# Optimization experiments

Measured on AMD Instinct MI355X. Metric: run time of the kernel, lower is better.

Reference implementation:

```python
import jax, jax.numpy as jnp
import numpy as np

LN_EPS = 1e-6

def _layernorm(x, g, b):
    mu = jnp.mean(x, axis=-1, keepdims=True)
    var = jnp.mean((x - mu) ** 2, axis=-1, keepdims=True)
    return (x - mu) / jnp.sqrt(var + LN_EPS) * g + b

def _mha(q, k, v, wq, bq, wk, bk, wv, bv, fc, fcb, ln_g, ln_b, n_head, d_k, d_v):
    # standard post-LN multi-head attention (residual + layernorm), eval mode (no dropout)
    b, lq, _ = q.shape
    bk_, lk, _ = k.shape
    residual = q
    qh = (q @ wq + bq).reshape(b, lq, n_head, d_k).transpose(0, 2, 1, 3)      # [b,h,lq,dk]
    kh = (k @ wk + bk).reshape(bk_, lk, n_head, d_k).transpose(0, 2, 1, 3)    # [bk,h,lk,dk]
    vh = (v @ wv + bv).reshape(bk_, lk, n_head, d_v).transpose(0, 2, 1, 3)    # [bk,h,lk,dv]
    attn = jax.nn.softmax(jnp.matmul(qh, kh.swapaxes(-1, -2)) / (d_k ** 0.5), axis=-1)  # [b,h,lq,lk]
    out = jnp.matmul(attn, vh)                                                # [b,h,lq,dv]
    out = out.transpose(0, 2, 1, 3).reshape(b, lq, n_head * d_v)
    pre = out
    out = _layernorm(out @ fc + fcb + residual, ln_g, ln_b)
    return out, attn, pre


def setup_inputs() -> dict:
    key = jax.random.key(0)
    ks = jax.random.split(key, 32)
    B, C, H, W = 16, 64, 32, 32
    NC, D = 5, 96  # num_classes, memory feature dim
    s = 0.05
    d = {
        'x': jax.random.normal(ks[0], (B, C, H, W), jnp.float32),
        'memory': jax.random.normal(ks[1], (NC, D), jnp.float32),
        'wb_w': jax.random.normal(ks[2], (C, NC), jnp.float32) * s,
        'wb_b': jnp.zeros((NC,), jnp.float32),
        # slf_attn: n_head=1, d_model=64, d_input_k=96, d_k=96, d_v=64
        'a1_wq': jax.random.normal(ks[3], (64, 96), jnp.float32) * s,
        'a1_bq': jnp.zeros((96,), jnp.float32),
        'a1_wk': jax.random.normal(ks[4], (96, 96), jnp.float32) * s,
        'a1_bk': jnp.zeros((96,), jnp.float32),
        'a1_wv': jax.random.normal(ks[5], (96, 64), jnp.float32) * s,
        'a1_bv': jnp.zeros((64,), jnp.float32),
        'a1_fc': jax.random.normal(ks[6], (64, 64), jnp.float32) * s,
        'a1_fcb': jnp.zeros((64,), jnp.float32),
        'a1_ln_g': jnp.ones((64,), jnp.float32),
        'a1_ln_b': jnp.zeros((64,), jnp.float32),
        # slf_attn1: n_head=4, d_model=64, d_input_k=64, d_k=64, d_v=64
        'a2_wq': jax.random.normal(ks[7], (64, 256), jnp.float32) * s,
        'a2_bq': jnp.zeros((256,), jnp.float32),
        'a2_wk': jax.random.normal(ks[8], (64, 256), jnp.float32) * s,
        'a2_bk': jnp.zeros((256,), jnp.float32),
        'a2_wv': jax.random.normal(ks[9], (64, 256), jnp.float32) * s,
        'a2_bv': jnp.zeros((256,), jnp.float32),
        'a2_fc': jax.random.normal(ks[10], (256, 64), jnp.float32) * s,
        'a2_fcb': jnp.zeros((64,), jnp.float32),
        'a2_ln_g': jnp.ones((64,), jnp.float32),
        'a2_ln_b': jnp.zeros((64,), jnp.float32),
    }
    return d


def reference(x, memory, wb_w, wb_b,
              a1_wq, a1_bq, a1_wk, a1_bk, a1_wv, a1_bv, a1_fc, a1_fcb, a1_ln_g, a1_ln_b,
              a2_wq, a2_bq, a2_wk, a2_bk, a2_wv, a2_bv, a2_fc, a2_fcb, a2_ln_g, a2_ln_b):
    b, c, H, W = x.shape
    xt = x.transpose(0, 2, 3, 1).reshape(b, H * W, c)            # [b,HW,64]
    weight = xt @ wb_w + wb_b                                    # [b,HW,5]
    weight1 = jax.nn.softmax(weight, axis=-1)                    # softmax over classes
    weight2 = jax.nn.softmax(weight.transpose(0, 2, 1), axis=-1) # [b,5,HW], softmax over HW
    class_feat1 = jnp.matmul(weight2, xt)                        # [b,5,64] class-weighted pooling
    mem = memory[None]                                           # [1,5,96]
    cf, _, _ = _mha(class_feat1, mem, mem,
                    a1_wq, a1_bq, a1_wk, a1_bk, a1_wv, a1_bv, a1_fc, a1_fcb, a1_ln_g, a1_ln_b,
                    n_head=1, d_k=96, d_v=64)                    # [b,5,64]
    cf = jnp.matmul(weight1, cf)                                 # redistribution [b,HW,64]
    cf, _, _ = _mha(cf, cf, cf,
                    a2_wq, a2_bq, a2_wk, a2_bk, a2_wv, a2_bv, a2_fc, a2_fcb, a2_ln_g, a2_ln_b,
                    n_head=4, d_k=64, d_v=64)                    # [b,HW,64]
    return cf.transpose(0, 2, 1).reshape(-1, 64, H, W)           # [b,64,H,W]
```

## Files before the change

kernel.cpp:

```cpp
#include <hip/hip_runtime.h>
#include <math.h>

typedef unsigned short ushort_t;
typedef __attribute__((ext_vector_type(8))) short short8;
typedef __attribute__((ext_vector_type(4))) float f32x4;

#define B_  16
#define HW_ 1024
#define C_  64
#define NC_ 5
#define D1_ 96
#define NH_ 4
#define DH_ 64

#define MFMA32(A,B,C) __builtin_amdgcn_mfma_f32_16x16x32_bf16(A,B,C,0,0,0)

__device__ __forceinline__ ushort_t f2bf(float f) {
    unsigned u = __float_as_uint(f);
    u = u + 0x7fffu + ((u >> 16) & 1u);
    return (ushort_t)(u >> 16);
}

__device__ __forceinline__ unsigned pack2_trunc(float lo, float hi) {
    return (__float_as_uint(hi) & 0xffff0000u) | (__float_as_uint(lo) >> 16);
}
__device__ __forceinline__ unsigned pack2_rne(float lo, float hi) {
    return ((unsigned)f2bf(hi) << 16) | (unsigned)f2bf(lo);
}
__device__ __forceinline__ float bf_lo(unsigned u) { return __uint_as_float(u << 16); }
__device__ __forceinline__ float bf_hi(unsigned u) { return __uint_as_float(u & 0xffff0000u); }

__device__ __forceinline__ void gload16(const ushort_t* g, ushort_t* l) {
    __builtin_amdgcn_global_load_lds(
        (const __attribute__((address_space(1))) unsigned int*)g,
        (__attribute__((address_space(3))) unsigned int*)l,
        16, 0, 0);
}

__global__ __launch_bounds__(256) void k0_fcT(const float* __restrict__ fc,
                                              ushort_t* __restrict__ F) {
    int c = blockIdx.x * 256 + threadIdx.x;
    int l = c & 63, s = (c >> 6) & 7, n = c >> 9;
    int col = n * 16 + (l & 15);
    int k0 = s * 32 + (l >> 4) * 8;
    union { ushort_t us[8]; uint4 u; } pk;
#pragma unroll
    for (int j = 0; j < 8; j++) pk.us[j] = f2bf(fc[(k0 + j) * 64 + col]);
    *(uint4*)(F + (size_t)c * 8) = pk.u;
}

__global__ __launch_bounds__(256) void k1_logits(const float* __restrict__ x,
                                                 const float* __restrict__ wb_w,
                                                 const float* __restrict__ wb_b,
                                                 float* __restrict__ logitsT,
                                                 float* __restrict__ w1) {
    __shared__ float part[4][64][6];
    int t = threadIdx.x, w = t >> 6, lane = t & 63;
    int b = blockIdx.x >> 4;
    int hw = (blockIdx.x & 15) * 64 + lane;
    const float* xb = x + ((size_t)b * C_ + w * 16) * HW_;
    float acc[NC_] = {0.f, 0.f, 0.f, 0.f, 0.f};
#pragma unroll
    for (int c = 0; c < 16; c++) {
        float xv = xb[c * HW_ + hw];
        const float* wp = wb_w + (w * 16 + c) * NC_;
#pragma unroll
        for (int j = 0; j < NC_; j++) acc[j] += xv * wp[j];
    }
#pragma unroll
    for (int j = 0; j < NC_; j++) part[w][lane][j] = acc[j];
    __syncthreads();
    if (w == 0) {
        float a[NC_];
#pragma unroll
        for (int j = 0; j < NC_; j++)
            a[j] = wb_b[j] + acc[j] + part[1][lane][j] + part[2][lane][j] + part[3][lane][j];
        float m = a[0];
#pragma unroll
        for (int j = 1; j < NC_; j++) m = fmaxf(m, a[j]);
        float e[NC_], s = 0.f;
#pragma unroll
        for (int j = 0; j < NC_; j++) { e[j] = __expf(a[j] - m); s += e[j]; }
        float inv = 1.f / s;
        int idx = b * HW_ + hw;
#pragma unroll
        for (int j = 0; j < NC_; j++) {
            logitsT[((size_t)b * NC_ + j) * HW_ + hw] = a[j];
            w1[(size_t)idx * NC_ + j] = e[j] * inv;
        }
    }
}

__global__ __launch_bounds__(256) void k2b_pool(const float* __restrict__ x,
                                                const float* __restrict__ logitsT,
                                                float* __restrict__ cf1) {
    __shared__ float pl[NC_ * HW_];
    __shared__ float sinv[NC_];
    int t = threadIdx.x;
    int b = blockIdx.x >> 4, chg = blockIdx.x & 15;
    const float* lp = logitsT + (size_t)b * NC_ * HW_;
    for (int i = t * 4; i < NC_ * HW_; i += 1024)
        *(float4*)(pl + i) = *(const float4*)(lp + i);
    __syncthreads();
    int w = t >> 6, lane = t & 63;
    for (int r = w; r < NC_; r += 4) {
        float m = -1e30f;
        for (int i = lane; i < HW_; i += 64) m = fmaxf(m, pl[r * HW_ + i]);
#pragma unroll
        for (int off = 1; off < 64; off <<= 1) m = fmaxf(m, __shfl_xor(m, off, 64));
        float s = 0.f;
        for (int i = lane; i < HW_; i += 64) {
            float e = __expf(pl[r * HW_ + i] - m);
            pl[r * HW_ + i] = e;
            s += e;
        }
#pragma unroll
        for (int off = 1; off < 64; off <<= 1) s += __shfl_xor(s, off, 64);
        if (lane == 0) sinv[r] = 1.f / s;
    }
    __syncthreads();
    int ch = chg * 4 + w;
    const float* xc = x + ((size_t)b * C_ + ch) * HW_;
    float acc[NC_] = {0.f, 0.f, 0.f, 0.f, 0.f};
#pragma unroll
    for (int i = 0; i < HW_ / 64; i++) {
        int hw = i * 64 + lane;
        float xv = xc[hw];
#pragma unroll
        for (int c = 0; c < NC_; c++) acc[c] += xv * pl[c * HW_ + hw];
    }
#pragma unroll
    for (int c = 0; c < NC_; c++) {
        float a = acc[c];
#pragma unroll
        for (int off = 1; off < 64; off <<= 1) a += __shfl_xor(a, off, 64);
        if (lane == 0) cf1[((size_t)b * NC_ + c) * C_ + ch] = a * sinv[c];
    }
}

__global__ __launch_bounds__(256) void k3_mha1(const float* __restrict__ cf1,
                                               const float* __restrict__ wq, const float* __restrict__ bq,
                                               const float* __restrict__ mem,
                                               const float* __restrict__ wk, const float* __restrict__ bk,
                                               const float* __restrict__ wv, const float* __restrict__ bv,
                                               const float* __restrict__ fc, const float* __restrict__ fcb,
                                               const float* __restrict__ lng, const float* __restrict__ lnb,
                                               float* __restrict__ cfs) {
    __shared__ float cs[NC_ * C_];
    __shared__ float kh[NC_ * D1_];
    __shared__ float vh[NC_ * DH_];
    __shared__ float q[NC_ * D1_];
    __shared__ float sc[NC_ * NC_];
    __shared__ float pp[NC_ * NC_];
    __shared__ float o[NC_ * C_];
    __shared__ float z[NC_ * C_];
    __shared__ float mu[NC_], rs[NC_];
    int t = threadIdx.x, b = blockIdx.x;
    for (int i = t; i < NC_ * C_; i += 256) cs[i] = cf1[(size_t)b * NC_ * C_ + i];
    for (int idx = t; idx < NC_ * D1_; idx += 256) {
        int i = idx / D1_, k = idx % D1_;
        float a = bk[k];
        for (int d = 0; d < D1_; d++) a += mem[i * D1_ + d] * wk[d * D1_ + k];
        kh[idx] = a;
    }
    for (int idx = t; idx < NC_ * DH_; idx += 256) {
        int i = idx / DH_, dv = idx % DH_;
        float a = bv[dv];
        for (int d = 0; d < D1_; d++) a += mem[i * D1_ + d] * wv[d * DH_ + dv];
        vh[idx] = a;
    }
    __syncthreads();
    for (int idx = t; idx < NC_ * D1_; idx += 256) {
        int i = idx / D1_, k = idx % D1_;
        float a = bq[k];
        for (int c = 0; c < C_; c++) a += cs[i * C_ + c] * wq[c * D1_ + k];
        q[idx] = a;
    }
    __syncthreads();
    if (t < NC_ * NC_) {
        int i = t / NC_, j = t % NC_;
        float a = 0.f;
        for (int k = 0; k < D1_; k++) a += q[i * D1_ + k] * kh[j * D1_ + k];
        sc[t] = a * 0.1020620726159657f;
    }
    __syncthreads();
    if (t < NC_) {
        float m = sc[t * NC_];
        for (int j = 1; j < NC_; j++) m = fmaxf(m, sc[t * NC_ + j]);
        float e[NC_], s = 0.f;
        for (int j = 0; j < NC_; j++) { e[j] = __expf(sc[t * NC_ + j] - m); s += e[j]; }
        float inv = 1.f / s;
        for (int j = 0; j < NC_; j++) pp[t * NC_ + j] = e[j] * inv;
    }
    __syncthreads();
    for (int idx = t; idx < NC_ * C_; idx += 256) {
        int i = idx / C_, dv = idx % C_;
        float a = 0.f;
        for (int j = 0; j < NC_; j++) a += pp[i * NC_ + j] * vh[j * C_ + dv];
        o[idx] = a;
    }
    __syncthreads();
    for (int idx = t; idx < NC_ * C_; idx += 256) {
        int i = idx / C_, dd = idx % C_;
        float a = fcb[dd] + cs[idx];
        for (int c2 = 0; c2 < C_; c2++) a += o[i * C_ + c2] * fc[c2 * C_ + dd];
        z[idx] = a;
    }
    __syncthreads();
    if (t < NC_) {
        float s = 0.f;
        for (int d = 0; d < C_; d++) s += z[t * C_ + d];
        float mm = s / C_;
        float v = 0.f;
        for (int d = 0; d < C_; d++) { float dd2 = z[t * C_ + d] - mm; v += dd2 * dd2; }
        mu[t] = mm; rs[t] = rsqrtf(v / C_ + 1e-6f);
    }
    __syncthreads();
    for (int idx = t; idx < NC_ * C_; idx += 256) {
        int i = idx / C_, dd = idx % C_;
        cfs[(size_t)b * NC_ * C_ + idx] = (z[idx] - mu[i]) * rs[i] * lng[dd] + lnb[dd];
    }
}

__global__ __launch_bounds__(256) void k5_mfma(const float* __restrict__ w1,
                                               const float* __restrict__ cfs,
                                               const float* __restrict__ wq, const float* __restrict__ bq,
                                               const float* __restrict__ wk, const float* __restrict__ bk,
                                               const float* __restrict__ wv, const float* __restrict__ bv,
                                               ushort_t* __restrict__ Qb, ushort_t* __restrict__ Kb,
                                               ushort_t* __restrict__ Vt) {
    __shared__ ushort_t Af[64][68];
    __shared__ ushort_t Wt[256][68];
    int t = threadIdx.x;
    int which = blockIdx.y;
    int m0 = blockIdx.x * 64;
    int b = m0 >> 10, lbase = m0 & 1023;
    {
        int r = t >> 2, ks = (t & 3) * 16;
        const float* cp = cfs + (size_t)b * NC_ * C_;
        const float* w1p = w1 + (size_t)(m0 + r) * NC_;
        float v0 = w1p[0], v1 = w1p[1], v2 = w1p[2], v3 = w1p[3], v4 = w1p[4];
#pragma unroll
        for (int j = 0; j < 16; j += 2) {
            int k = ks + j;
            float e0 = v0 * cp[k]       + v1 * cp[64 + k]     + v2 * cp[128 + k]
                     + v3 * cp[192 + k] + v4 * cp[256 + k];
            float e1 = v0 * cp[k + 1]     + v1 * cp[64 + k + 1] + v2 * cp[128 + k + 1]
                     + v3 * cp[192 + k + 1] + v4 * cp[256 + k + 1];
            *(unsigned*)&Af[r][k] = pack2_rne(e0, e1);
        }
    }
    const float* W = (which == 0) ? wq : (which == 1) ? wk : wv;
    {
        int n = t;
#pragma unroll
        for (int k = 0; k < 64; k += 2) {
            *(unsigned*)&Wt[n][k] = pack2_rne(W[k * 256 + n], W[(k + 1) * 256 + n]);
        }
    }
    __syncthreads();
    int lane = t & 63, w = t >> 6;
    int l15 = lane & 15, quad = lane >> 4;
    if (which < 2) {
        const float* bias = (which == 0) ? bq : bk;
        float scale = (which == 0) ? 0.18033688011112042f : 1.0f;
        ushort_t* dst = (which == 0) ? Qb : Kb;
        short8 a0[4], a1[4];
#pragma unroll
        for (int mi = 0; mi < 4; mi++) {
            a0[mi] = *(const short8*)&Af[mi * 16 + l15][quad * 8];
            a1[mi] = *(const short8*)&Af[mi * 16 + l15][32 + quad * 8];
        }
#pragma unroll
        for (int nt = 0; nt < 4; nt++) {
            int ni = w * 4 + nt;
            short8 b0 = *(const short8*)&Wt[ni * 16 + l15][quad * 8];
            short8 b1 = *(const short8*)&Wt[ni * 16 + l15][32 + quad * 8];
            int n = ni * 16 + l15;
            float bb = bias[n];
            int h = n >> 6, dd = n & 63;
#pragma unroll
            for (int mi = 0; mi < 4; mi++) {
                f32x4 z = {0, 0, 0, 0};
                f32x4 dv4 = MFMA32(a0[mi], b0, z);
                dv4 = MFMA32(a1[mi], b1, dv4);
                size_t base = ((size_t)(b * NH_ + h) * HW_ + (lbase + mi * 16 + quad * 4)) * DH_ + dd;
#pragma unroll
                for (int r = 0; r < 4; r++)
                    dst[base + (size_t)r * DH_] = f2bf((dv4[r] + bb) * scale);
            }
        }
    } else {
        short8 a0[4], a1[4];
#pragma unroll
        for (int mt = 0; mt < 4; mt++) {
            int mi = w * 4 + mt;
            a0[mt] = *(const short8*)&Wt[mi * 16 + l15][quad * 8];
            a1[mt] = *(const short8*)&Wt[mi * 16 + l15][32 + quad * 8];
        }
#pragma unroll
        for (int nt = 0; nt < 4; nt++) {
            short8 b0 = *(const short8*)&Af[nt * 16 + l15][quad * 8];
            short8 b1 = *(const short8*)&Af[nt * 16 + l15][32 + quad * 8];
#pragma unroll
            for (int mt = 0; mt < 4; mt++) {
                int mi = w * 4 + mt;
                f32x4 z = {0, 0, 0, 0};
                f32x4 dv4 = MFMA32(a0[mt], b0, z);
                dv4 = MFMA32(a1[mt], b1, dv4);
                int h = mi >> 2;
#pragma unroll
                for (int r = 0; r < 4; r++) {
                    int nw = mi * 16 + quad * 4 + r;
                    int dv = nw & 63;
                    Vt[((size_t)(b * NH_ + h) * DH_ + dv) * HW_ + lbase + nt * 16 + l15] =
                        f2bf(dv4[r] + bv[nw]);
                }
            }
        }
    }
}

__global__ __launch_bounds__(256) void k6_attn(const ushort_t* __restrict__ Qb,
                                               const ushort_t* __restrict__ Kb,
                                               const ushort_t* __restrict__ Vt,
                                               ushort_t* __restrict__ aoP0, ushort_t* __restrict__ aoP1,
                                               float* __restrict__ sP0, float* __restrict__ sP1) {
    __shared__ ushort_t Kst[2][8][512];
    int t = threadIdx.x;
    int w = t >> 6;
    int lane = t & 63;
    int l15 = lane & 15;
    int quad = lane >> 4;
    int L = blockIdx.x;
    int bh = ((L >> 3) & 7) * 8 + (L & 7);
    int khalf = (L >> 6) & 1;
    int qt = L >> 7;
    int b = bh >> 2, h = bh & 3;
    const ushort_t* Qp = Qb + (size_t)bh * HW_ * DH_;
    const ushort_t* Kp = Kb + (size_t)bh * HW_ * DH_;
    const ushort_t* Vp = Vt + (size_t)bh * DH_ * HW_;
    int row0 = qt * 256 + w * 16;
    short8 q0[4], q1[4];
#pragma unroll
    for (int tl = 0; tl < 4; tl++) {
        const ushort_t* qp = Qp + (size_t)(row0 + tl * 64 + l15) * DH_ + quad * 8;
        q0[tl] = *(const short8*)(qp);
        q1[tl] = *(const short8*)(qp + 32);
    }
    int f0 = ((l15 >> 2) * 8) + (l15 & 3);
    int kstart = khalf * 512;
    const ushort_t* K0p = Kp + (size_t)(kstart + f0) * DH_ + quad * 8;
    const ushort_t* K1p = Kp + (size_t)(kstart + f0 + 4) * DH_ + quad * 8;
    const ushort_t* Vp0 = Vp + (size_t)(0 * 16 + l15) * HW_ + kstart + quad * 8;
    const ushort_t* Vp1 = Vp + (size_t)(1 * 16 + l15) * HW_ + kstart + quad * 8;
    const ushort_t* Vp2 = Vp + (size_t)(2 * 16 + l15) * HW_ + kstart + quad * 8;
    const ushort_t* Vp3 = Vp + (size_t)(3 * 16 + l15) * HW_ + kstart + quad * 8;
    auto stage = [&](int kt, int bb) {
        size_t koff = (size_t)kt * 32 * DH_;
        int kb32 = kt * 32;
        if (w == 0) {
            gload16(K0p + koff,      &Kst[bb][0][0]);
            gload16(K0p + koff + 32, &Kst[bb][1][0]);
        } else if (w == 1) {
            gload16(K1p + koff,      &Kst[bb][2][0]);
            gload16(K1p + koff + 32, &Kst[bb][3][0]);
        } else if (w == 2) {
            gload16(Vp0 + kb32, &Kst[bb][4][0]);
            gload16(Vp1 + kb32, &Kst[bb][5][0]);
        } else {
            gload16(Vp2 + kb32, &Kst[bb][6][0]);
            gload16(Vp3 + kb32, &Kst[bb][7][0]);
        }
    };
    const short ONE = (short)0x3F80;
    short8 ones = {ONE, ONE, ONE, ONE, ONE, ONE, ONE, ONE};
    f32x4 o0[4], o1[4], o2[4], o3[4], oS[4];
#pragma unroll
    for (int tl = 0; tl < 4; tl++) {
        o0[tl] = (f32x4){0,0,0,0}; o1[tl] = (f32x4){0,0,0,0};
        o2[tl] = (f32x4){0,0,0,0}; o3[tl] = (f32x4){0,0,0,0};
        oS[tl] = (f32x4){0,0,0,0};
    }
    stage(0, 0);
    for (int kt = 0; kt < 16; kt++) {
        int bb = kt & 1;
        __syncthreads();
        if (kt < 15) stage(kt + 1, bb ^ 1);
        const ushort_t* S = &Kst[bb][0][0];
        short8 ka0 = *(const short8*)(S + 0 * 512 + lane * 8);
        short8 ka1 = *(const short8*)(S + 1 * 512 + lane * 8);
        short8 kb0 = *(const short8*)(S + 2 * 512 + lane * 8);
        short8 kb1 = *(const short8*)(S + 3 * 512 + lane * 8);
        short8 v0  = *(const short8*)(S + 4 * 512 + lane * 8);
        short8 v1  = *(const short8*)(S + 5 * 512 + lane * 8);
        short8 v2  = *(const short8*)(S + 6 * 512 + lane * 8);
        short8 v3  = *(const short8*)(S + 7 * 512 + lane * 8);
        f32x4 z = {0,0,0,0};
#pragma unroll
        for (int tl = 0; tl < 4; tl++) {
            f32x4 s0 = MFMA32(ka0, q0[tl], z);  s0 = MFMA32(ka1, q1[tl], s0);
            f32x4 s1 = MFMA32(kb0, q0[tl], z);  s1 = MFMA32(kb1, q1[tl], s1);
            float p0 = exp2f(s0[0]), p1 = exp2f(s0[1]), p2 = exp2f(s0[2]), p3 = exp2f(s0[3]);
            float p4 = exp2f(s1[0]), p5 = exp2f(s1[1]), p6 = exp2f(s1[2]), p7 = exp2f(s1[3]);
            union { short8 v; unsigned u[4]; } pf;
            pf.u[0] = pack2_trunc(p0, p1);  pf.u[1] = pack2_trunc(p2, p3);
            pf.u[2] = pack2_trunc(p4, p5);  pf.u[3] = pack2_trunc(p6, p7);
            o0[tl] = MFMA32(v0, pf.v, o0[tl]);
            o1[tl] = MFMA32(v1, pf.v, o1[tl]);
            o2[tl] = MFMA32(v2, pf.v, o2[tl]);
            o3[tl] = MFMA32(v3, pf.v, o3[tl]);
            oS[tl] = MFMA32(ones, pf.v, oS[tl]);
        }
    }
    ushort_t* aoP = khalf ? aoP1 : aoP0;
    float* sP = khalf ? sP1 : sP0;
#pragma unroll
    for (int tl = 0; tl < 4; tl++) {
        int rowg = row0 + tl * 64 + l15;
        ushort_t* aop = aoP + ((size_t)(b * HW_ + rowg)) * 256 + h * 64 + quad * 4;
        uint2 u;
        u.x = pack2_trunc(o0[tl][0], o0[tl][1]); u.y = pack2_trunc(o0[tl][2], o0[tl][3]);
        *(uint2*)(aop + 0) = u;
        u.x = pack2_trunc(o1[tl][0], o1[tl][1]); u.y = pack2_trunc(o1[tl][2], o1[tl][3]);
        *(uint2*)(aop + 16) = u;
        u.x = pack2_trunc(o2[tl][0], o2[tl][1]); u.y = pack2_trunc(o2[tl][2], o2[tl][3]);
        *(uint2*)(aop + 32) = u;
        u.x = pack2_trunc(o3[tl][0], o3[tl][1]); u.y = pack2_trunc(o3[tl][2], o3[tl][3]);
        *(uint2*)(aop + 48) = u;
        if (quad == 0)
            sP[(size_t)(b * HW_ + rowg) * NH_ + h] = oS[tl][0];
    }
}

__global__ __launch_bounds__(256) void k7_final(const ushort_t* __restrict__ aoP0,
                                                const ushort_t* __restrict__ aoP1,
                                                const float* __restrict__ sP0,
                                                const float* __restrict__ sP1,
                                                const float* __restrict__ w1,
                                                const float* __restrict__ cfs,
                                                const ushort_t* __restrict__ F,
                                                const float* __restrict__ fcb,
                                                const float* __restrict__ lng, const float* __restrict__ lnb,
                                                float* __restrict__ out) {
    __shared__ ushort_t Afr[512 * 8];
    __shared__ float rinv[64];
    __shared__ float T[16][68];
    __shared__ float To[64 * 17];
    int t = threadIdx.x, w = t >> 6, lane = t & 63;
    int m0 = blockIdx.x * 16, b = m0 >> 10;
    if (t < 64) {
        int row = t >> 2, hh = t & 3;
        float s = sP0[(size_t)(m0 + row) * NH_ + hh] + sP1[(size_t)(m0 + row) * NH_ + hh];
        rinv[t] = 1.f / s;
    }
    __syncthreads();
#pragma unroll
    for (int cc = t; cc < 512; cc += 256) {
        int s = cc >> 6, l = cc & 63;
        int row = l & 15, col0 = s * 32 + (l >> 4) * 8;
        int hh = col0 >> 6;
        size_t base = (size_t)(m0 + row) * 256 + col0;
        uint4 a = *(const uint4*)(aoP0 + base);
        uint4 c4 = *(const uint4*)(aoP1 + base);
        float r = rinv[row * 4 + hh];
        uint4 pk;
        pk.x = pack2_trunc((bf_lo(a.x) + bf_lo(c4.x)) * r, (bf_hi(a.x) + bf_hi(c4.x)) * r);
        pk.y = pack2_trunc((bf_lo(a.y) + bf_lo(c4.y)) * r, (bf_hi(a.y) + bf_hi(c4.y)) * r);
        pk.z = pack2_trunc((bf_lo(a.z) + bf_lo(c4.z)) * r, (bf_hi(a.z) + bf_hi(c4.z)) * r);
        pk.w = pack2_trunc((bf_lo(a.w) + bf_lo(c4.w)) * r, (bf_hi(a.w) + bf_hi(c4.w)) * r);
        *(uint4*)&Afr[(size_t)cc * 8] = pk;
    }
    __syncthreads();
    f32x4 acc = {0, 0, 0, 0};
#pragma unroll
    for (int s = 0; s < 8; s++) {
        short8 a = *(const short8*)&Afr[(s * 64 + lane) * 8];
        short8 bf8 = *(const short8*)(F + ((size_t)(w * 8 + s) * 64 + lane) * 8);
        acc = MFMA32(a, bf8, acc);
    }
    {
        int l15 = lane & 15, quad = lane >> 4;
#pragma unroll
        for (int r = 0; r < 4; r++) T[quad * 4 + r][w * 16 + l15] = acc[r];
    }
    __syncthreads();
    int d = lane;
    float g = lng[d], be = lnb[d], bias = fcb[d];
    const float* cp = cfs + (size_t)b * NC_ * C_;
#pragma unroll
    for (int j = 0; j < 4; j++) {
        int row = w * 4 + j;
        const float* w1p = w1 + (size_t)(m0 + row) * NC_;
        float a = bias + T[row][d];
#pragma unroll
        for (int c = 0; c < NC_; c++) a += w1p[c] * cp[c * 64 + d];
        float s1 = a, s2 = a * a;
#pragma unroll
        for (int off = 1; off < 64; off <<= 1) {
            s1 += __shfl_xor(s1, off, 64);
            s2 += __shfl_xor(s2, off, 64);
        }
        float mu = s1 * (1.f / 64.f);
        float var = s2 * (1.f / 64.f) - mu * mu;
        float rstd = rsqrtf(var + 1e-6f);
        To[d * 17 + row] = (a - mu) * rstd * g + be;
    }
    __syncthreads();
    int ch = t >> 2, part = t & 3;
    int hw0 = m0 & 1023;
    float4 v = {To[ch * 17 + part * 4 + 0], To[ch * 17 + part * 4 + 1],
                To[ch * 17 + part * 4 + 2], To[ch * 17 + part * 4 + 3]};
    *(float4*)&out[((size_t)b * 64 + ch) * 1024 + hw0 + part * 4] = v;
}

extern "C" void kernel_launch(void* const* d_in, const int* in_sizes, int n_in,
                              void* d_out, int out_size, void* d_ws, size_t ws_size,
                              hipStream_t stream) {
    const float* x      = (const float*)d_in[0];
    const float* memory = (const float*)d_in[1];
    const float* wb_w   = (const float*)d_in[2];
    const float* wb_b   = (const float*)d_in[3];
    const float* a1_wq  = (const float*)d_in[4];
    const float* a1_bq  = (const float*)d_in[5];
    const float* a1_wk  = (const float*)d_in[6];
    const float* a1_bk  = (const float*)d_in[7];
    const float* a1_wv  = (const float*)d_in[8];
    const float* a1_bv  = (const float*)d_in[9];
    const float* a1_fc  = (const float*)d_in[10];
    const float* a1_fcb = (const float*)d_in[11];
    const float* a1_ln_g = (const float*)d_in[12];
    const float* a1_ln_b = (const float*)d_in[13];
    const float* a2_wq  = (const float*)d_in[14];
    const float* a2_bq  = (const float*)d_in[15];
    const float* a2_wk  = (const float*)d_in[16];
    const float* a2_bk  = (const float*)d_in[17];
    const float* a2_wv  = (const float*)d_in[18];
    const float* a2_bv  = (const float*)d_in[19];
    const float* a2_fc  = (const float*)d_in[20];
    const float* a2_fcb = (const float*)d_in[21];
    const float* a2_ln_g = (const float*)d_in[22];
    const float* a2_ln_b = (const float*)d_in[23];

    float* ws = (float*)d_ws;
    float* logitsT = ws;
    float* w1  = logitsT + 81920;
    float* cf1 = w1 + 81920;
    float* cfs = cf1 + 5120;
    float* sP0 = cfs + 5120;
    float* sP1 = sP0 + 65536;
    ushort_t* aoP0 = (ushort_t*)(sP1 + 65536);
    ushort_t* aoP1 = aoP0 + 4194304;
    ushort_t* Qb = aoP1 + 4194304;
    ushort_t* Kb = Qb + 4194304;
    ushort_t* Vt = Kb + 4194304;
    ushort_t* F  = Vt + 4194304;

    k0_fcT<<<8, 256, 0, stream>>>(a2_fc, F);
    k1_logits<<<256, 256, 0, stream>>>(x, wb_w, wb_b, logitsT, w1);
    k2b_pool<<<256, 256, 0, stream>>>(x, logitsT, cf1);
    k3_mha1<<<16, 256, 0, stream>>>(cf1, a1_wq, a1_bq, memory, a1_wk, a1_bk,
                                    a1_wv, a1_bv, a1_fc, a1_fcb,
                                    a1_ln_g, a1_ln_b, cfs);
    k5_mfma<<<dim3(256, 3), 256, 0, stream>>>(w1, cfs, a2_wq, a2_bq, a2_wk, a2_bk,
                                              a2_wv, a2_bv, Qb, Kb, Vt);
    k6_attn<<<512, 256, 0, stream>>>(Qb, Kb, Vt, aoP0, aoP1, sP0, sP1);
    k7_final<<<1024, 256, 0, stream>>>(aoP0, aoP1, sP0, sP1, w1, cfs, F, a2_fcb,
                                       a2_ln_g, a2_ln_b, (float*)d_out);
}
```

Before: 187.0 us.

## Split attention keys into four chunks and fold small prep kernels into logits launch

The attention kernel now splits the key dimension into four quarters instead of two, doubling the grid to 1024 blocks so more CUs are busy. Each block handles half as many key tiles. The final kernel sums four partial outputs and softmax denominators instead of two. Separately, the fc transpose kernel and the memory K/V projections (previously recomputed in every k3 block) are folded into extra blocks of the logits launch, removing one launch and redundant work. This costs twice the partial-output write and read traffic in the combine step.

```diff
diff --git a/kernel.cpp b/kernel.cpp
--- a/kernel.cpp
+++ b/kernel.cpp
@@ -37,25 +37,47 @@
         16, 0, 0);
 }
 
-__global__ __launch_bounds__(256) void k0_fcT(const float* __restrict__ fc,
-                                              ushort_t* __restrict__ F) {
-    int c = blockIdx.x * 256 + threadIdx.x;
-    int l = c & 63, s = (c >> 6) & 7, n = c >> 9;
-    int col = n * 16 + (l & 15);
-    int k0 = s * 32 + (l >> 4) * 8;
-    union { ushort_t us[8]; uint4 u; } pk;
-#pragma unroll
-    for (int j = 0; j < 8; j++) pk.us[j] = f2bf(fc[(k0 + j) * 64 + col]);
-    *(uint4*)(F + (size_t)c * 8) = pk.u;
-}
-
 __global__ __launch_bounds__(256) void k1_logits(const float* __restrict__ x,
                                                  const float* __restrict__ wb_w,
                                                  const float* __restrict__ wb_b,
+                                                 const float* __restrict__ fc2,
+                                                 const float* __restrict__ mem,
+                                                 const float* __restrict__ wk, const float* __restrict__ bk,
+                                                 const float* __restrict__ wv, const float* __restrict__ bv,
                                                  float* __restrict__ logitsT,
-                                                 float* __restrict__ w1) {
+                                                 float* __restrict__ w1,
+                                                 ushort_t* __restrict__ F,
+                                                 float* __restrict__ khG, float* __restrict__ vhG) {
+    int t = threadIdx.x;
+    if (blockIdx.x >= 256) {
+        int xb2 = blockIdx.x - 256;
+        if (xb2 < 8) {
+            int c = xb2 * 256 + t;
+            int l = c & 63, s = (c >> 6) & 7, n = c >> 9;
+            int col = n * 16 + (l & 15);
+            int k0 = s * 32 + (l >> 4) * 8;
+            union { ushort_t us[8]; uint4 u; } pk;
+#pragma unroll
+            for (int j = 0; j < 8; j++) pk.us[j] = f2bf(fc2[(k0 + j) * 64 + col]);
+            *(uint4*)(F + (size_t)c * 8) = pk.u;
+        } else {
+            for (int idx = t; idx < NC_ * D1_; idx += 256) {
+                int i = idx / D1_, k = idx % D1_;
+                float a = bk[k];
+                for (int d = 0; d < D1_; d++) a += mem[i * D1_ + d] * wk[d * D1_ + k];
+                khG[idx] = a;
+            }
+            for (int idx = t; idx < NC_ * DH_; idx += 256) {
+                int i = idx / DH_, dv = idx % DH_;
+                float a = bv[dv];
+                for (int d = 0; d < D1_; d++) a += mem[i * D1_ + d] * wv[d * DH_ + dv];
+                vhG[idx] = a;
+            }
+        }
+        return;
+    }
     __shared__ float part[4][64][6];
-    int t = threadIdx.x, w = t >> 6, lane = t & 63;
+    int w = t >> 6, lane = t & 63;
     int b = blockIdx.x >> 4;
     int hw = (blockIdx.x & 15) * 64 + lane;
     const float* xb = x + ((size_t)b * C_ + w * 16) * HW_;
@@ -140,9 +162,7 @@
 
 __global__ __launch_bounds__(256) void k3_mha1(const float* __restrict__ cf1,
                                                const float* __restrict__ wq, const float* __restrict__ bq,
-                                               const float* __restrict__ mem,
-                                               const float* __restrict__ wk, const float* __restrict__ bk,
-                                               const float* __restrict__ wv, const float* __restrict__ bv,
+                                               const float* __restrict__ khG, const float* __restrict__ vhG,
                                                const float* __restrict__ fc, const float* __restrict__ fcb,
                                                const float* __restrict__ lng, const float* __restrict__ lnb,
                                                float* __restrict__ cfs) {
@@ -157,18 +177,8 @@
     __shared__ float mu[NC_], rs[NC_];
     int t = threadIdx.x, b = blockIdx.x;
     for (int i = t; i < NC_ * C_; i += 256) cs[i] = cf1[(size_t)b * NC_ * C_ + i];
-    for (int idx = t; idx < NC_ * D1_; idx += 256) {
-        int i = idx / D1_, k = idx % D1_;
-        float a = bk[k];
-        for (int d = 0; d < D1_; d++) a += mem[i * D1_ + d] * wk[d * D1_ + k];
-        kh[idx] = a;
-    }
-    for (int idx = t; idx < NC_ * DH_; idx += 256) {
-        int i = idx / DH_, dv = idx % DH_;
-        float a = bv[dv];
-        for (int d = 0; d < D1_; d++) a += mem[i * D1_ + d] * wv[d * DH_ + dv];
-        vh[idx] = a;
-    }
+    for (int idx = t; idx < NC_ * D1_; idx += 256) kh[idx] = khG[idx];
+    for (int idx = t; idx < NC_ * DH_; idx += 256) vh[idx] = vhG[idx];
     __syncthreads();
     for (int idx = t; idx < NC_ * D1_; idx += 256) {
         int i = idx / D1_, k = idx % D1_;
@@ -324,8 +334,8 @@
 __global__ __launch_bounds__(256) void k6_attn(const ushort_t* __restrict__ Qb,
                                                const ushort_t* __restrict__ Kb,
                                                const ushort_t* __restrict__ Vt,
-                                               ushort_t* __restrict__ aoP0, ushort_t* __restrict__ aoP1,
-                                               float* __restrict__ sP0, float* __restrict__ sP1) {
+                                               ushort_t* __restrict__ aoPb,
+                                               float* __restrict__ sPb) {
     __shared__ ushort_t Kst[2][8][512];
     int t = threadIdx.x;
     int w = t >> 6;
@@ -334,8 +344,9 @@
     int quad = lane >> 4;
     int L = blockIdx.x;
     int bh = ((L >> 3) & 7) * 8 + (L & 7);
-    int khalf = (L >> 6) & 1;
-    int qt = L >> 7;
+    int r2 = L >> 6;
+    int kq = r2 & 3;
+    int qt = r2 >> 2;
     int b = bh >> 2, h = bh & 3;
     const ushort_t* Qp = Qb + (size_t)bh * HW_ * DH_;
     const ushort_t* Kp = Kb + (size_t)bh * HW_ * DH_;
@@ -349,7 +360,7 @@
         q1[tl] = *(const short8*)(qp + 32);
     }
     int f0 = ((l15 >> 2) * 8) + (l15 & 3);
-    int kstart = khalf * 512;
+    int kstart = kq * 256;
     const ushort_t* K0p = Kp + (size_t)(kstart + f0) * DH_ + quad * 8;
     const ushort_t* K1p = Kp + (size_t)(kstart + f0 + 4) * DH_ + quad * 8;
     const ushort_t* Vp0 = Vp + (size_t)(0 * 16 + l15) * HW_ + kstart + quad * 8;
@@ -383,10 +394,10 @@
         oS[tl] = (f32x4){0,0,0,0};
     }
     stage(0, 0);
-    for (int kt = 0; kt < 16; kt++) {
+    for (int kt = 0; kt < 8; kt++) {
         int bb = kt & 1;
         __syncthreads();
-        if (kt < 15) stage(kt + 1, bb ^ 1);
+        if (kt < 7) stage(kt + 1, bb ^ 1);
         const ushort_t* S = &Kst[bb][0][0];
         short8 ka0 = *(const short8*)(S + 0 * 512 + lane * 8);
         short8 ka1 = *(const short8*)(S + 1 * 512 + lane * 8);
@@ -413,8 +424,8 @@
             oS[tl] = MFMA32(ones, pf.v, oS[tl]);
         }
     }
-    ushort_t* aoP = khalf ? aoP1 : aoP0;
-    float* sP = khalf ? sP1 : sP0;
+    ushort_t* aoP = aoPb + (size_t)kq * 4194304;
+    float* sP = sPb + (size_t)kq * 65536;
 #pragma unroll
     for (int tl = 0; tl < 4; tl++) {
         int rowg = row0 + tl * 64 + l15;
@@ -433,10 +444,8 @@
     }
 }
 
-__global__ __launch_bounds__(256) void k7_final(const ushort_t* __restrict__ aoP0,
-                                                const ushort_t* __restrict__ aoP1,
-                                                const float* __restrict__ sP0,
-                                                const float* __restrict__ sP1,
+__global__ __launch_bounds__(256) void k7_final(const ushort_t* __restrict__ aoPb,
+                                                const float* __restrict__ sPb,
                                                 const float* __restrict__ w1,
                                                 const float* __restrict__ cfs,
                                                 const ushort_t* __restrict__ F,
@@ -451,7 +460,8 @@
     int m0 = blockIdx.x * 16, b = m0 >> 10;
     if (t < 64) {
         int row = t >> 2, hh = t & 3;
-        float s = sP0[(size_t)(m0 + row) * NH_ + hh] + sP1[(size_t)(m0 + row) * NH_ + hh];
+        size_t si = (size_t)(m0 + row) * NH_ + hh;
+        float s = sPb[si] + sPb[65536 + si] + sPb[2 * 65536 + si] + sPb[3 * 65536 + si];
         rinv[t] = 1.f / s;
     }
     __syncthreads();
@@ -461,14 +471,20 @@
         int row = l & 15, col0 = s * 32 + (l >> 4) * 8;
         int hh = col0 >> 6;
         size_t base = (size_t)(m0 + row) * 256 + col0;
-        uint4 a = *(const uint4*)(aoP0 + base);
-        uint4 c4 = *(const uint4*)(aoP1 + base);
+        uint4 a0 = *(const uint4*)(aoPb + base);
+        uint4 a1 = *(const uint4*)(aoPb + 4194304 + base);
+        uint4 a2 = *(const uint4*)(aoPb + 2 * 4194304 + base);
+        uint4 a3 = *(const uint4*)(aoPb + 3 * 4194304 + base);
         float r = rinv[row * 4 + hh];
         uint4 pk;
-        pk.x = pack2_trunc((bf_lo(a.x) + bf_lo(c4.x)) * r, (bf_hi(a.x) + bf_hi(c4.x)) * r);
-        pk.y = pack2_trunc((bf_lo(a.y) + bf_lo(c4.y)) * r, (bf_hi(a.y) + bf_hi(c4.y)) * r);
-        pk.z = pack2_trunc((bf_lo(a.z) + bf_lo(c4.z)) * r, (bf_hi(a.z) + bf_hi(c4.z)) * r);
-        pk.w = pack2_trunc((bf_lo(a.w) + bf_lo(c4.w)) * r, (bf_hi(a.w) + bf_hi(c4.w)) * r);
+        pk.x = pack2_trunc((bf_lo(a0.x) + bf_lo(a1.x) + bf_lo(a2.x) + bf_lo(a3.x)) * r,
+                           (bf_hi(a0.x) + bf_hi(a1.x) + bf_hi(a2.x) + bf_hi(a3.x)) * r);
+        pk.y = pack2_trunc((bf_lo(a0.y) + bf_lo(a1.y) + bf_lo(a2.y) + bf_lo(a3.y)) * r,
+                           (bf_hi(a0.y) + bf_hi(a1.y) + bf_hi(a2.y) + bf_hi(a3.y)) * r);
+        pk.z = pack2_trunc((bf_lo(a0.z) + bf_lo(a1.z) + bf_lo(a2.z) + bf_lo(a3.z)) * r,
+                           (bf_hi(a0.z) + bf_hi(a1.z) + bf_hi(a2.z) + bf_hi(a3.z)) * r);
+        pk.w = pack2_trunc((bf_lo(a0.w) + bf_lo(a1.w) + bf_lo(a2.w) + bf_lo(a3.w)) * r,
+                           (bf_hi(a0.w) + bf_hi(a1.w) + bf_hi(a2.w) + bf_hi(a3.w)) * r);
         *(uint4*)&Afr[(size_t)cc * 8] = pk;
     }
     __syncthreads();
@@ -547,24 +563,24 @@
     float* w1  = logitsT + 81920;
     float* cf1 = w1 + 81920;
     float* cfs = cf1 + 5120;
-    float* sP0 = cfs + 5120;
-    float* sP1 = sP0 + 65536;
-    ushort_t* aoP0 = (ushort_t*)(sP1 + 65536);
-    ushort_t* aoP1 = aoP0 + 4194304;
-    ushort_t* Qb = aoP1 + 4194304;
+    float* khG = cfs + 5120;
+    float* vhG = khG + 480;
+    float* sPb = vhG + 320;
+    ushort_t* aoPb = (ushort_t*)(sPb + 4 * 65536);
+    ushort_t* Qb = aoPb + 4 * 4194304;
     ushort_t* Kb = Qb + 4194304;
     ushort_t* Vt = Kb + 4194304;
     ushort_t* F  = Vt + 4194304;
 
-    k0_fcT<<<8, 256, 0, stream>>>(a2_fc, F);
-    k1_logits<<<256, 256, 0, stream>>>(x, wb_w, wb_b, logitsT, w1);
+    k1_logits<<<265, 256, 0, stream>>>(x, wb_w, wb_b, a2_fc, memory,
+                                       a1_wk, a1_bk, a1_wv, a1_bv,
+                                       logitsT, w1, F, khG, vhG);
     k2b_pool<<<256, 256, 0, stream>>>(x, logitsT, cf1);
-    k3_mha1<<<16, 256, 0, stream>>>(cf1, a1_wq, a1_bq, memory, a1_wk, a1_bk,
-                                    a1_wv, a1_bv, a1_fc, a1_fcb,
+    k3_mha1<<<16, 256, 0, stream>>>(cf1, a1_wq, a1_bq, khG, vhG, a1_fc, a1_fcb,
                                     a1_ln_g, a1_ln_b, cfs);
     k5_mfma<<<dim3(256, 3), 256, 0, stream>>>(w1, cfs, a2_wq, a2_bq, a2_wk, a2_bk,
                                               a2_wv, a2_bv, Qb, Kb, Vt);
-    k6_attn<<<512, 256, 0, stream>>>(Qb, Kb, Vt, aoP0, aoP1, sP0, sP1);
-    k7_final<<<1024, 256, 0, stream>>>(aoP0, aoP1, sP0, sP1, w1, cfs, F, a2_fcb,
+    k6_attn<<<1024, 256, 0, stream>>>(Qb, Kb, Vt, aoPb, sPb);
+    k7_final<<<1024, 256, 0, stream>>>(aoPb, sPb, w1, cfs, F, a2_fcb,
                                        a2_ln_g, a2_ln_b, (float*)d_out);
 }
```

Measured after the change: 189.6 us. Within noise of the previous version (+1.4%).
